# Kernel optimization log

Measured on AMD Instinct MI355X. Metric: run time of the kernel, lower is better.

## Reference

```python
import jax, jax.numpy as jnp
import numpy as np

H = 2048      # hidden_size
NH = 16       # num_heads
HD = H // NH  # head_dim
B, T = 2, 2048


def setup_inputs() -> dict:
    key = jax.random.key(0)
    ks = jax.random.split(key, 5)
    s = 1.0 / np.sqrt(H)
    return {
        "x": jax.random.normal(ks[0], (B, T, H), dtype=jnp.float32),
        "wq": jax.random.normal(ks[1], (H, H), dtype=jnp.float32) * s,
        "bq": jnp.zeros((H,), dtype=jnp.float32),
        "wk": jax.random.normal(ks[2], (H, H), dtype=jnp.float32) * s,
        "bk": jnp.zeros((H,), dtype=jnp.float32),
        "wv": jax.random.normal(ks[3], (H, H), dtype=jnp.float32) * s,
        "bv": jnp.zeros((H,), dtype=jnp.float32),
        "wo": jax.random.normal(ks[4], (H, H), dtype=jnp.float32) * s,
        "bo": jnp.zeros((H,), dtype=jnp.float32),
    }


def reference(x, wq, bq, wk, bk, wv, bv, wo, bo):
    Bx, Tx, C = x.shape
    # projections (torch Linear: x @ W.T + b)
    q = x @ wq.T + bq
    k = x @ wk.T + bk
    v = x @ wv.T + bv
    # [B, T, H] -> [B, NH, T, HD]
    q = q.reshape(Bx, Tx, NH, HD).transpose(0, 2, 1, 3)
    k = k.reshape(Bx, Tx, NH, HD).transpose(0, 2, 1, 3)
    v = v.reshape(Bx, Tx, NH, HD).transpose(0, 2, 1, 3)
    scale = 1.0 / np.sqrt(HD).astype(np.float32)
    scores = jnp.einsum('bhqd,bhkd->bhqk', q, k) * scale  # [B, NH, T, T]
    causal = jnp.tril(jnp.ones((Tx, Tx), dtype=bool))
    scores = jnp.where(causal[None, None], scores, -jnp.inf)
    attn = jax.nn.softmax(scores, axis=-1)
    out = jnp.einsum('bhqk,bhkd->bhqd', attn, v)  # [B, NH, T, HD]
    out = out.transpose(0, 2, 1, 3).reshape(Bx, Tx, C)
    return out @ wo.T + bo
```

## Files before the change

kernel.cpp:

```cpp
#include <hip/hip_runtime.h>
#include <stdint.h>

constexpr int H_  = 2048;
constexpr int NH_ = 16;
constexpr int HD_ = 128;
constexpr int B_  = 2;
constexpr int T_  = 2048;
constexpr int M_  = B_ * T_;

typedef unsigned short u16;
typedef __bf16 bf16x8 __attribute__((ext_vector_type(8)));
typedef float  f32x4  __attribute__((ext_vector_type(4)));

constexpr float C1_ = 0.08838834764831845f * 1.4426950408889634f;

template <int N> struct IC { static constexpr int value = N; };

__device__ __forceinline__ u16 f2bf(float f) {
  uint32_t u = __builtin_bit_cast(uint32_t, f);
  u += 0x7fffu + ((u >> 16) & 1u);
  return (u16)(u >> 16);
}

__device__ __forceinline__ uint32_t cvtpk(float lo, float hi) {
  uint32_t r;
  asm("v_cvt_pk_bf16_f32 %0, %1, %2" : "=v"(r) : "v"(lo), "v"(hi));
  return r;
}

__device__ __forceinline__ void gload_lds16(const void* g, void* lds) {
  auto gp = (const __attribute__((address_space(1))) uint32_t*)(uintptr_t)g;
  auto lp = (__attribute__((address_space(3))) uint32_t*)(uint32_t)(uintptr_t)lds;
  __builtin_amdgcn_global_load_lds(gp, lp, 16, 0, 0);
}

__device__ __forceinline__ f32x4 mfma16(bf16x8 a, bf16x8 b, f32x4 c) {
  return __builtin_amdgcn_mfma_f32_16x16x32_bf16(a, b, c, 0, 0, 0);
}

__global__ __launch_bounds__(512) void cvt5_kernel(
    const float4* __restrict__ x,  const float4* __restrict__ wq,
    const float4* __restrict__ wk, const float4* __restrict__ wv,
    const float4* __restrict__ wo, ushort4* __restrict__ dst) {
  const int bid = blockIdx.x, tid = threadIdx.x;
  const float4* src;
  size_t idx, dof;
  if (bid < 4096) {
    src = x; idx = (size_t)bid * 512 + tid; dof = 0;
  } else {
    int w = (bid - 4096) >> 11;
    int r = (bid - 4096) & 2047;
    idx = (size_t)r * 512 + tid;
    dof = 2097152u + (size_t)w * 1048576u;
    src = (w == 0) ? wq : (w == 1) ? wk : (w == 2) ? wv : wo;
  }
  float4 v = src[idx];
  ushort4 o;
  o.x = f2bf(v.x); o.y = f2bf(v.y); o.z = f2bf(v.z); o.w = f2bf(v.w);
  dst[dof + idx] = o;
}

__device__ __forceinline__ void gemm256_core(const u16* __restrict__ A,
                                             const u16* __restrict__ Bm,
                                             const float* __restrict__ bias,
                                             void* __restrict__ Cout,
                                             int bid, int outmode,
                                             float oscale) {
  __shared__ u16 As[2][256 * 64];
  __shared__ u16 Bs[2][128 * 64];
  constexpr int Kg = H_;
  constexpr int NT = Kg / 64;
  const int tid = threadIdx.x;
  const int wave = tid >> 6, lane = tid & 63, l15 = lane & 15, lhi = lane >> 4;
  const int tm = bid & 15, tn = bid >> 4;
  const int m0 = tm << 8, n0 = tn << 7;
  const int wr = wave >> 1, wc = wave & 1;

  f32x4 acc[4][4] = {};

  auto stageA = [&](int kt, int buf, int a) {
    int o = a * 8192 + tid * 16;
    int row = o >> 7;
    int sw = o ^ ((row & 7) << 4);
    int c8 = (sw >> 4) & 7;
    gload_lds16(A + (size_t)(m0 + row) * Kg + kt * 64 + c8 * 8,
                (char*)&As[buf][0] + a * 8192 + wave * 1024);
  };
  auto stageB = [&](int kt, int buf, int a) {
    int o = a * 8192 + tid * 16;
    int row = o >> 7;
    int sw = o ^ ((row & 7) << 4);
    int c8 = (sw >> 4) & 7;
    gload_lds16(Bm + (size_t)(n0 + row) * Kg + kt * 64 + c8 * 8,
                (char*)&Bs[buf][0] + a * 8192 + wave * 1024);
  };
  auto rdA = [&](int buf, int kk, int mi) -> bf16x8 {
    int row = wr * 64 + mi * 16 + l15;
    int ob = (row * 128 + kk * 64 + lhi * 16) ^ ((row & 7) << 4);
    return *(const bf16x8*)((const char*)&As[buf][0] + ob);
  };
  auto rdB = [&](int buf, int kk, int ni) -> bf16x8 {
    int row = wc * 64 + ni * 16 + l15;
    int ob = (row * 128 + kk * 64 + lhi * 16) ^ ((row & 7) << 4);
    return *(const bf16x8*)((const char*)&Bs[buf][0] + ob);
  };

  stageB(0, 0, 0); stageB(0, 0, 1);
  stageA(0, 0, 0); stageA(0, 0, 1); stageA(0, 0, 2); stageA(0, 0, 3);
  asm volatile("s_waitcnt vmcnt(0)" ::: "memory");
  __builtin_amdgcn_s_barrier();
  asm volatile("" ::: "memory");

  int cur = 0;
  for (int kt = 0; kt < NT; ++kt) {
    const bool hn = (kt + 1 < NT);
    bf16x8 a0, a1, b0, b1, b2, b3;

    a0 = rdA(cur, 0, 0); a1 = rdA(cur, 0, 1);
    b0 = rdB(cur, 0, 0); b1 = rdB(cur, 0, 1);
    b2 = rdB(cur, 0, 2); b3 = rdB(cur, 0, 3);
    if (hn) { stageB(kt + 1, cur ^ 1, 0); stageB(kt + 1, cur ^ 1, 1); }
    __builtin_amdgcn_s_barrier(); asm volatile("" ::: "memory");
    __builtin_amdgcn_s_setprio(1);
    acc[0][0] = mfma16(a0, b0, acc[0][0]); acc[0][1] = mfma16(a0, b1, acc[0][1]);
    acc[0][2] = mfma16(a0, b2, acc[0][2]); acc[0][3] = mfma16(a0, b3, acc[0][3]);
    acc[1][0] = mfma16(a1, b0, acc[1][0]); acc[1][1] = mfma16(a1, b1, acc[1][1]);
    acc[1][2] = mfma16(a1, b2, acc[1][2]); acc[1][3] = mfma16(a1, b3, acc[1][3]);
    __builtin_amdgcn_s_setprio(0);
    __builtin_amdgcn_s_barrier(); asm volatile("" ::: "memory");

    a0 = rdA(cur, 0, 2); a1 = rdA(cur, 0, 3);
    if (hn) { stageA(kt + 1, cur ^ 1, 0); stageA(kt + 1, cur ^ 1, 1); }
    __builtin_amdgcn_s_barrier(); asm volatile("" ::: "memory");
    __builtin_amdgcn_s_setprio(1);
    acc[2][0] = mfma16(a0, b0, acc[2][0]); acc[2][1] = mfma16(a0, b1, acc[2][1]);
    acc[2][2] = mfma16(a0, b2, acc[2][2]); acc[2][3] = mfma16(a0, b3, acc[2][3]);
    acc[3][0] = mfma16(a1, b0, acc[3][0]); acc[3][1] = mfma16(a1, b1, acc[3][1]);
    acc[3][2] = mfma16(a1, b2, acc[3][2]); acc[3][3] = mfma16(a1, b3, acc[3][3]);
    __builtin_amdgcn_s_setprio(0);
    __builtin_amdgcn_s_barrier(); asm volatile("" ::: "memory");

    a0 = rdA(cur, 1, 0); a1 = rdA(cur, 1, 1);
    b0 = rdB(cur, 1, 0); b1 = rdB(cur, 1, 1);
    b2 = rdB(cur, 1, 2); b3 = rdB(cur, 1, 3);
    if (hn) { stageA(kt + 1, cur ^ 1, 2); stageA(kt + 1, cur ^ 1, 3); }
    __builtin_amdgcn_s_barrier(); asm volatile("" ::: "memory");
    __builtin_amdgcn_s_setprio(1);
    acc[0][0] = mfma16(a0, b0, acc[0][0]); acc[0][1] = mfma16(a0, b1, acc[0][1]);
    acc[0][2] = mfma16(a0, b2, acc[0][2]); acc[0][3] = mfma16(a0, b3, acc[0][3]);
    acc[1][0] = mfma16(a1, b0, acc[1][0]); acc[1][1] = mfma16(a1, b1, acc[1][1]);
    acc[1][2] = mfma16(a1, b2, acc[1][2]); acc[1][3] = mfma16(a1, b3, acc[1][3]);
    __builtin_amdgcn_s_setprio(0);
    __builtin_amdgcn_s_barrier(); asm volatile("" ::: "memory");

    a0 = rdA(cur, 1, 2); a1 = rdA(cur, 1, 3);
    __builtin_amdgcn_s_barrier(); asm volatile("" ::: "memory");
    __builtin_amdgcn_s_setprio(1);
    acc[2][0] = mfma16(a0, b0, acc[2][0]); acc[2][1] = mfma16(a0, b1, acc[2][1]);
    acc[2][2] = mfma16(a0, b2, acc[2][2]); acc[2][3] = mfma16(a0, b3, acc[2][3]);
    acc[3][0] = mfma16(a1, b0, acc[3][0]); acc[3][1] = mfma16(a1, b1, acc[3][1]);
    acc[3][2] = mfma16(a1, b2, acc[3][2]); acc[3][3] = mfma16(a1, b3, acc[3][3]);
    __builtin_amdgcn_s_setprio(0);
    asm volatile("s_waitcnt vmcnt(0)" ::: "memory");
    __builtin_amdgcn_s_barrier(); asm volatile("" ::: "memory");
    cur ^= 1;
  }

  float bv[4];
#pragma unroll
  for (int ni = 0; ni < 4; ++ni) bv[ni] = bias[n0 + wc * 64 + ni * 16 + l15];

  if (outmode == 2) {
    const int b = m0 >> 11;
    const int tbase = (m0 & 2047) + wr * 64 + lhi * 4;
#pragma unroll
    for (int mi = 0; mi < 4; ++mi) {
#pragma unroll
      for (int ni = 0; ni < 4; ++ni) {
        int n = n0 + wc * 64 + ni * 16 + l15;
        ushort4 pk;
        pk.x = f2bf(acc[mi][ni][0] + bv[ni]);
        pk.y = f2bf(acc[mi][ni][1] + bv[ni]);
        pk.z = f2bf(acc[mi][ni][2] + bv[ni]);
        pk.w = f2bf(acc[mi][ni][3] + bv[ni]);
        *(ushort4*)((u16*)Cout + (size_t)(b * 2048 + n) * T_ + tbase +
                    mi * 16) = pk;
      }
    }
  } else {
#pragma unroll
    for (int mi = 0; mi < 4; ++mi) {
#pragma unroll
      for (int ni = 0; ni < 4; ++ni) {
        int n = n0 + wc * 64 + ni * 16 + l15;
#pragma unroll
        for (int r = 0; r < 4; ++r) {
          int m = m0 + wr * 64 + mi * 16 + lhi * 4 + r;
          float v = (acc[mi][ni][r] + bv[ni]) * oscale;
          if (outmode == 1)
            ((float*)Cout)[(size_t)m * H_ + n] = v;
          else
            ((u16*)Cout)[(size_t)m * H_ + n] = f2bf(v);
        }
      }
    }
  }
}

template <int OUTMODE>
__global__ __launch_bounds__(512, 2) void gemm256_bt_k(
    const u16* __restrict__ A, const u16* __restrict__ Bm,
    const float* __restrict__ bias, void* __restrict__ Cout, float oscale) {
  gemm256_core(A, Bm, bias, Cout, blockIdx.x, OUTMODE, oscale);
}

__global__ __launch_bounds__(256, 2) void attn_kernel(
    const u16* __restrict__ Q, const u16* __restrict__ K,
    const u16* __restrict__ Vt, u16* __restrict__ ctx) {
  __shared__ u16 Ks[2][64 * 128];
  __shared__ u16 Vs[2][128 * 64];
  __shared__ u16 Ps[4][1024];

  const int tid = threadIdx.x, wave = tid >> 6, lane = tid & 63;
  const int l15 = lane & 15, lhi = lane >> 4;

  const int bid = blockIdx.x;
  const int xcd = bid & 7, idx = bid >> 3;
  const int bh = xcd * 4 + (idx & 3);
  const int qi = idx >> 2;
  const int b = bh >> 4, h = bh & 15;
  const int qb0 = qi, qb1 = 31 - qi;
  const int bt = qb0 + 1;

  const float THR = 11.5f;
  const float NI  = -__builtin_inff();

  auto stage = [&](auto bufc, int kv0) {
    constexpr int BUF = decltype(bufc)::value;
#pragma unroll
    for (int is = 0; is < 4; ++is) {
      {
        int o_ = is * 4096 + tid * 16;
        int row = o_ >> 8;
        int sw = o_ ^ (((o_ >> 8) & 7) << 4);
        int c8 = (sw >> 4) & 15;
        gload_lds16(K + (size_t)(b * T_ + kv0 + row) * H_ + h * HD_ + c8 * 8,
                    &Ks[BUF][0] + (is * 2048 + wave * 512));
      }
      {
        int o_ = is * 4096 + tid * 16;
        int row = o_ >> 7;
        int sw = o_ ^ (((o_ >> 7) & 7) << 4);
        int t8 = (sw >> 4) & 7;
        gload_lds16(Vt + (size_t)(bh * HD_ + row) * T_ + kv0 + t8 * 8,
                    &Vs[BUF][0] + (is * 4096 / 2 + wave * 512));
      }
    }
  };

  bf16x8 qc[4], qn[4];
  {
    const u16* q0p =
        Q + (size_t)(b * T_ + qb0 * 64 + wave * 16 + l15) * H_ + h * HD_ + lhi * 8;
    const u16* q1p =
        Q + (size_t)(b * T_ + qb1 * 64 + wave * 16 + l15) * H_ + h * HD_ + lhi * 8;
#pragma unroll
    for (int kk = 0; kk < 4; ++kk) {
      qc[kk] = *(const bf16x8*)(q0p + kk * 32);
      qn[kk] = *(const bf16x8*)(q1p + kk * 32);
    }
  }

  f32x4 o[8] = {};
  float m2 = NI, lr = 0.f;

  auto flushout = [&](int qtile) {
    float invo[4];
    float inv = 1.0f / lr;
#pragma unroll
    for (int r = 0; r < 4; ++r) invo[r] = __shfl(inv, lhi * 4 + r);
    int q0 = qtile * 64 + wave * 16;
#pragma unroll
    for (int dt = 0; dt < 8; ++dt)
#pragma unroll
      for (int r = 0; r < 4; ++r)
        ctx[(size_t)(b * T_ + q0 + lhi * 4 + r) * H_ + h * HD_ + dt * 16 +
            l15] = f2bf(o[dt][r] * invo[r]);
  };

  stage(IC<0>{}, 0);
  asm volatile("s_waitcnt vmcnt(0)" ::: "memory");
  __builtin_amdgcn_s_barrier();
  asm volatile("" ::: "memory");

  auto body = [&](int t, auto bufc) {
    constexpr int BUF = decltype(bufc)::value;
    if (t < 32) {
      int tn = t + 1;
      int kvn = ((tn >= bt) ? tn - bt : tn) * 64;
      stage(IC<BUF ^ 1>{}, kvn);
    }
    if (t == bt) {
      flushout(qb0);
#pragma unroll
      for (int dt = 0; dt < 8; ++dt) o[dt] = f32x4{0.f, 0.f, 0.f, 0.f};
      m2 = NI;
      lr = 0.f;
#pragma unroll
      for (int kk = 0; kk < 4; ++kk) qc[kk] = qn[kk];
    }
    if (t < 32)
      asm volatile("s_waitcnt vmcnt(8)" ::: "memory");
    else
      asm volatile("s_waitcnt vmcnt(0)" ::: "memory");
    __builtin_amdgcn_s_barrier();
    asm volatile("" ::: "memory");

    const int kvt = (t >= bt) ? t - bt : t;
    const int kv0 = kvt * 64;
    const int qtile = (t >= bt) ? qb1 : qb0;
    const int q0 = qtile * 64 + wave * 16;
    const int qrow = q0 + l15;

    f32x4 sv[4];
    __builtin_amdgcn_s_setprio(1);
#pragma unroll
    for (int kt = 0; kt < 4; ++kt) {
      f32x4 sacc = {0.f, 0.f, 0.f, 0.f};
#pragma unroll
      for (int kk = 0; kk < 4; ++kk) {
        int row = kt * 16 + l15;
        int ob = (row * 256 + kk * 64 + lhi * 16) ^ ((row & 7) << 4);
        bf16x8 kf = *(const bf16x8*)((const char*)&Ks[BUF][0] + ob);
        sacc = mfma16(kf, qc[kk], sacc);
      }
      sv[kt] = sacc;
    }
    __builtin_amdgcn_s_setprio(0);

    float pmax2 = NI;
    const bool diag = (t == qb0) || (t == 32);
    if (diag) {
#pragma unroll
      for (int kt = 0; kt < 4; ++kt)
#pragma unroll
        for (int r = 0; r < 4; ++r) {
          int key = kv0 + kt * 16 + lhi * 4 + r;
          float z = (key <= qrow) ? sv[kt][r] : NI;
          sv[kt][r] = z;
          pmax2 = fmaxf(pmax2, z);
        }
    } else {
#pragma unroll
      for (int kt = 0; kt < 4; ++kt)
#pragma unroll
        for (int r = 0; r < 4; ++r) pmax2 = fmaxf(pmax2, sv[kt][r]);
    }
    pmax2 = fmaxf(pmax2, __shfl_xor(pmax2, 16));
    pmax2 = fmaxf(pmax2, __shfl_xor(pmax2, 32));

    if (__any(pmax2 - m2 > THR)) {
      float mn = fmaxf(m2, pmax2);
      float al = exp2f(m2 - mn);
      m2 = mn;
      lr *= al;
      float alo[4];
#pragma unroll
      for (int r = 0; r < 4; ++r) alo[r] = __shfl(al, lhi * 4 + r);
#pragma unroll
      for (int dt = 0; dt < 8; ++dt)
#pragma unroll
        for (int r = 0; r < 4; ++r) o[dt][r] *= alo[r];
    }

    float rs = 0.f;
#pragma unroll
    for (int kt = 0; kt < 4; ++kt)
#pragma unroll
      for (int r = 0; r < 4; ++r) {
        float p = exp2f(sv[kt][r] - m2);
        sv[kt][r] = p;
        rs += p;
      }
    rs += __shfl_xor(rs, 16);
    rs += __shfl_xor(rs, 32);
    lr += rs;

#pragma unroll
    for (int kt = 0; kt < 4; ++kt) {
      int slot = kt * 2 + (lhi >> 1);
      uint2 pk;
      pk.x = cvtpk(sv[kt][0], sv[kt][1]);
      pk.y = cvtpk(sv[kt][2], sv[kt][3]);
      *(uint2*)&Ps[wave][slot * 128 + ((l15 * 8) ^ ((slot & 7) << 3)) +
                         (lhi & 1) * 4] = pk;
    }
    asm volatile("" ::: "memory");

    __builtin_amdgcn_s_setprio(1);
#pragma unroll
    for (int ks = 0; ks < 2; ++ks) {
      int slot = ks * 4 + lhi;
      bf16x8 pf = *(const bf16x8*)&Ps[wave][slot * 128 +
                                            ((l15 * 8) ^ ((slot & 7) << 3))];
#pragma unroll
      for (int dt = 0; dt < 8; ++dt) {
        int row = dt * 16 + l15;
        int ob = (row * 128 + ks * 64 + lhi * 16) ^ ((row & 7) << 4);
        bf16x8 vf = *(const bf16x8*)((const char*)&Vs[BUF][0] + ob);
        o[dt] = mfma16(pf, vf, o[dt]);
      }
    }
    __builtin_amdgcn_s_setprio(0);

    __builtin_amdgcn_s_barrier();
    asm volatile("" ::: "memory");
  };

#pragma unroll 1
  for (int t2 = 0; t2 < 32; t2 += 2) {
    body(t2, IC<0>{});
    body(t2 + 1, IC<1>{});
  }
  body(32, IC<0>{});
  flushout(qb1);
}

extern "C" void kernel_launch(void* const* d_in, const int* in_sizes, int n_in,
                              void* d_out, int out_size, void* d_ws,
                              size_t ws_size, hipStream_t stream) {
  const float* x  = (const float*)d_in[0];
  const float* wq = (const float*)d_in[1];
  const float* bq = (const float*)d_in[2];
  const float* wk = (const float*)d_in[3];
  const float* bk = (const float*)d_in[4];
  const float* wv = (const float*)d_in[5];
  const float* bv = (const float*)d_in[6];
  const float* wo = (const float*)d_in[7];
  const float* bo = (const float*)d_in[8];

  char* ws = (char*)d_ws;
  constexpr size_t SZ_X = (size_t)M_ * H_ * 2;
  constexpr size_t SZ_W = (size_t)H_ * H_ * 2;
  u16* xb  = (u16*)(ws);
  u16* wqb = (u16*)(ws + SZ_X);
  u16* wkb = (u16*)(ws + SZ_X + 1 * SZ_W);
  u16* wvb = (u16*)(ws + SZ_X + 2 * SZ_W);
  u16* wob = (u16*)(ws + SZ_X + 3 * SZ_W);
  u16* Qb  = (u16*)(ws + 1 * SZ_X + 4 * SZ_W);
  u16* Kb  = (u16*)(ws + 2 * SZ_X + 4 * SZ_W);
  u16* Vtb = (u16*)(ws + 3 * SZ_X + 4 * SZ_W);
  u16* ctx = xb;

  cvt5_kernel<<<12288, 512, 0, stream>>>((const float4*)x, (const float4*)wq,
                                         (const float4*)wk, (const float4*)wv,
                                         (const float4*)wo, (ushort4*)ws);

  gemm256_bt_k<0><<<256, 512, 0, stream>>>(xb, wqb, bq, Qb, C1_);
  gemm256_bt_k<0><<<256, 512, 0, stream>>>(xb, wkb, bk, Kb, 1.0f);
  gemm256_bt_k<2><<<256, 512, 0, stream>>>(xb, wvb, bv, Vtb, 1.0f);

  attn_kernel<<<512, 256, 0, stream>>>(Qb, Kb, Vtb, ctx);

  gemm256_bt_k<1><<<256, 512, 0, stream>>>(ctx, wob, bo, d_out, 1.0f);
}
```

Measured before the change: 243.8 us.

## Single-buffer attention K/V tiles and raise occupancy to four blocks per CU

Replaces the double-buffered K/V shared-memory staging in the attention kernel with a single buffer and raises the launch bound from 2 to 4 blocks per CU. Each iteration now loads a tile, waits for all loads, computes, then synchronizes, so the prefetch overlap within a block is gone. The intent is to hide memory latency through more resident blocks and lower LDS use instead of in-block pipelining. The tighter register budget from the higher occupancy target may cause spills.

Result: slower. 296.6 us (+21.7%).

```diff
diff --git a/kernel.cpp b/kernel.cpp
--- a/kernel.cpp
+++ b/kernel.cpp
@@ -214,11 +214,11 @@
   gemm256_core(A, Bm, bias, Cout, blockIdx.x, OUTMODE, oscale);
 }
 
-__global__ __launch_bounds__(256, 2) void attn_kernel(
+__global__ __launch_bounds__(256, 4) void attn_kernel(
     const u16* __restrict__ Q, const u16* __restrict__ K,
     const u16* __restrict__ Vt, u16* __restrict__ ctx) {
-  __shared__ u16 Ks[2][64 * 128];
-  __shared__ u16 Vs[2][128 * 64];
+  __shared__ u16 Ks[64 * 128];
+  __shared__ u16 Vs[128 * 64];
   __shared__ u16 Ps[4][1024];
 
   const int tid = threadIdx.x, wave = tid >> 6, lane = tid & 63;
@@ -235,8 +235,7 @@
   const float THR = 11.5f;
   const float NI  = -__builtin_inff();
 
-  auto stage = [&](auto bufc, int kv0) {
-    constexpr int BUF = decltype(bufc)::value;
+  auto stage = [&](int kv0) {
 #pragma unroll
     for (int is = 0; is < 4; ++is) {
       {
@@ -245,7 +244,7 @@
         int sw = o_ ^ (((o_ >> 8) & 7) << 4);
         int c8 = (sw >> 4) & 15;
         gload_lds16(K + (size_t)(b * T_ + kv0 + row) * H_ + h * HD_ + c8 * 8,
-                    &Ks[BUF][0] + (is * 2048 + wave * 512));
+                    &Ks[0] + (is * 2048 + wave * 512));
       }
       {
         int o_ = is * 4096 + tid * 16;
@@ -253,7 +252,7 @@
         int sw = o_ ^ (((o_ >> 7) & 7) << 4);
         int t8 = (sw >> 4) & 7;
         gload_lds16(Vt + (size_t)(bh * HD_ + row) * T_ + kv0 + t8 * 8,
-                    &Vs[BUF][0] + (is * 4096 / 2 + wave * 512));
+                    &Vs[0] + (is * 2048 + wave * 512));
       }
     }
   };
@@ -288,18 +287,13 @@
             l15] = f2bf(o[dt][r] * invo[r]);
   };
 
-  stage(IC<0>{}, 0);
-  asm volatile("s_waitcnt vmcnt(0)" ::: "memory");
-  __builtin_amdgcn_s_barrier();
-  asm volatile("" ::: "memory");
-
-  auto body = [&](int t, auto bufc) {
-    constexpr int BUF = decltype(bufc)::value;
-    if (t < 32) {
-      int tn = t + 1;
-      int kvn = ((tn >= bt) ? tn - bt : tn) * 64;
-      stage(IC<BUF ^ 1>{}, kvn);
-    }
+#pragma unroll 1
+  for (int t = 0; t <= 32; ++t) {
+    const int kvt = (t >= bt) ? t - bt : t;
+    const int kv0 = kvt * 64;
+
+    stage(kv0);
+
     if (t == bt) {
       flushout(qb0);
 #pragma unroll
@@ -309,15 +303,11 @@
 #pragma unroll
       for (int kk = 0; kk < 4; ++kk) qc[kk] = qn[kk];
     }
-    if (t < 32)
-      asm volatile("s_waitcnt vmcnt(8)" ::: "memory");
-    else
-      asm volatile("s_waitcnt vmcnt(0)" ::: "memory");
+
+    asm volatile("s_waitcnt vmcnt(0)" ::: "memory");
     __builtin_amdgcn_s_barrier();
     asm volatile("" ::: "memory");
 
-    const int kvt = (t >= bt) ? t - bt : t;
-    const int kv0 = kvt * 64;
     const int qtile = (t >= bt) ? qb1 : qb0;
     const int q0 = qtile * 64 + wave * 16;
     const int qrow = q0 + l15;
@@ -331,7 +321,7 @@
       for (int kk = 0; kk < 4; ++kk) {
         int row = kt * 16 + l15;
         int ob = (row * 256 + kk * 64 + lhi * 16) ^ ((row & 7) << 4);
-        bf16x8 kf = *(const bf16x8*)((const char*)&Ks[BUF][0] + ob);
+        bf16x8 kf = *(const bf16x8*)((const char*)&Ks[0] + ob);
         sacc = mfma16(kf, qc[kk], sacc);
       }
       sv[kt] = sacc;
@@ -407,7 +397,7 @@
       for (int dt = 0; dt < 8; ++dt) {
         int row = dt * 16 + l15;
         int ob = (row * 128 + ks * 64 + lhi * 16) ^ ((row & 7) << 4);
-        bf16x8 vf = *(const bf16x8*)((const char*)&Vs[BUF][0] + ob);
+        bf16x8 vf = *(const bf16x8*)((const char*)&Vs[0] + ob);
         o[dt] = mfma16(pf, vf, o[dt]);
       }
     }
@@ -415,14 +405,7 @@
 
     __builtin_amdgcn_s_barrier();
     asm volatile("" ::: "memory");
-  };
-
-#pragma unroll 1
-  for (int t2 = 0; t2 < 32; t2 += 2) {
-    body(t2, IC<0>{});
-    body(t2 + 1, IC<1>{});
   }
-  body(32, IC<0>{});
   flushout(qb1);
 }
 
```
